# Kernel tuning notes

Hardware: AMD Instinct MI355X
Metric: run time of the kernel (lower is better)

Reference implementation:

```python
import jax, jax.numpy as jnp
import numpy as np

B, S, D_MODEL, D_K, D_V = 8, 2048, 1024, 1024, 1024


def setup_inputs() -> dict:
    key = jax.random.key(0)
    k1, k2, k3, k4 = jax.random.split(key, 4)
    x = jax.random.normal(k1, (B, S, D_MODEL), dtype=jnp.float32)
    # Store projection weights as [d_model, d_out] so projection is x @ W
    # (equivalent to torch Linear(d_model, d_out, bias=False) with W^T).
    scale = 1.0 / np.sqrt(D_MODEL)
    Wq = jax.random.normal(k2, (D_MODEL, D_K), dtype=jnp.float32) * scale
    Wk = jax.random.normal(k3, (D_MODEL, D_K), dtype=jnp.float32) * scale
    Wv = jax.random.normal(k4, (D_MODEL, D_V), dtype=jnp.float32) * scale
    return {"x": x, "Wq": Wq, "Wk": Wk, "Wv": Wv}


def reference(x, Wq, Wk, Wv):
    # Single-head causal self-attention, faithful to the original:
    # NOTE: the original scales by sqrt(x.shape[-1]) == sqrt(d_model),
    # not sqrt(d_k of the projection).
    Q = jnp.einsum('bsd,dk->bsk', x, Wq)
    K = jnp.einsum('bsd,dk->bsk', x, Wk)
    V = jnp.einsum('bsd,dv->bsv', x, Wv)
    inv_scale = 1.0 / jnp.sqrt(jnp.asarray(x.shape[-1], x.dtype))
    A = jnp.einsum('bqk,bsk->bqs', Q, K) * inv_scale  # [B, S, S]
    S_len = A.shape[-1]
    causal = jnp.tril(jnp.ones((S_len, S_len), dtype=bool))  # [S, S]
    A = jnp.where(causal, A, -jnp.inf)
    P = jax.nn.softmax(A, axis=-1)
    return jnp.einsum('bqs,bsv->bqv', P, V)
```

## Files before the change

kernel.cpp:

```cpp
#include <hip/hip_runtime.h>
#include <hip/hip_bf16.h>
#include <stdint.h>


typedef __bf16 bf16_t;
typedef __bf16 bf16x4 __attribute__((ext_vector_type(4)));
typedef __bf16 bf16x8 __attribute__((ext_vector_type(8)));
typedef float  floatx4 __attribute__((ext_vector_type(4)));

#define NB 8
#define SS 2048
#define DD 1024
#define INV_SCALE 0.03125f

__device__ __forceinline__ void async_ld16(const void* g, void* l) {
  __builtin_amdgcn_global_load_lds(
      (const __attribute__((address_space(1))) void*)g,
      (__attribute__((address_space(3))) void*)l, 16, 0, 0);
}

__device__ __forceinline__ void mm_core(const bf16_t* __restrict__ Ab,
                                        const bf16_t* __restrict__ Bb,
                                        int lda, int ldb, int kTiles,
                                        bf16_t* sA, bf16_t* sB,
                                        floatx4 acc[4][4]) {
  const int t    = threadIdx.x;
  const int lane = t & 63;
  const int wm   = (t >> 6) >> 1;
  const int wn   = (t >> 6) & 1;
  const int fm   = lane & 15;
  const int q    = lane >> 4;
  const int xo   = fm & 7;

  const bf16_t* ga[4]; const bf16_t* gb[4];
  bf16_t* la[4]; bf16_t* lb[4];
#pragma unroll
  for (int k = 0; k < 4; ++k) {
    const int u   = k * 256 + t;
    const int row = u >> 3;
    const int cc  = (u & 7) ^ (row & 7);
    ga[k] = Ab + (size_t)row * lda + cc * 8;
    gb[k] = Bb + (size_t)row * ldb + cc * 8;
    la[k] = sA + u * 8;
    lb[k] = sB + u * 8;
  }

  const bf16_t* pa = sA + (wm * 64 + fm) * 64;
  const bf16_t* pb = sB + (wn * 64 + fm) * 64;

  for (int kt = 0; kt < kTiles; ++kt) {
    const int ko = kt * 64;
#pragma unroll
    for (int k = 0; k < 4; ++k) async_ld16(ga[k] + ko, la[k]);
#pragma unroll
    for (int k = 0; k < 4; ++k) async_ld16(gb[k] + ko, lb[k]);
    __syncthreads();
#pragma unroll
    for (int h = 0; h < 2; ++h) {
      const int co = ((h * 4 + q) ^ xo) * 8;
      bf16x8 af[4], bfr[4];
#pragma unroll
      for (int i = 0; i < 4; ++i) af[i]  = *(const bf16x8*)(pa + i * 1024 + co);
#pragma unroll
      for (int j = 0; j < 4; ++j) bfr[j] = *(const bf16x8*)(pb + j * 1024 + co);
#pragma unroll
      for (int i = 0; i < 4; ++i)
#pragma unroll
        for (int j = 0; j < 4; ++j)
          acc[i][j] = __builtin_amdgcn_mfma_f32_16x16x32_bf16(bfr[j], af[i], acc[i][j], 0, 0, 0);
    }
    __syncthreads();
  }
}

__device__ __forceinline__ void zero_acc(floatx4 acc[4][4]) {
#pragma unroll
  for (int i = 0; i < 4; ++i)
#pragma unroll
    for (int j = 0; j < 4; ++j)
      acc[i][j] = floatx4{0.f, 0.f, 0.f, 0.f};
}


__global__ __launch_bounds__(256) void prep(const float* __restrict__ x,
                                            const float* __restrict__ Wq,
                                            const float* __restrict__ Wk,
                                            const float* __restrict__ Wv,
                                            bf16_t* __restrict__ xb,
                                            bf16_t* __restrict__ Wt) {
  __shared__ float tile[32][33];
  const int bid = blockIdx.x;
  const int t = threadIdx.x;
  if (bid < 16384) {
    size_t i = (size_t)bid * 256 + t;
    float4 v = ((const float4*)x)[i];
    bf16x4 o = {(bf16_t)v.x, (bf16_t)v.y, (bf16_t)v.z, (bf16_t)v.w};
    ((bf16x4*)xb)[i] = o;
  } else {
    const int wb = bid - 16384;
    const int z = wb >> 10;
    const int rem = wb & 1023;
    const float* W = (z == 0) ? Wq : (z == 1 ? Wk : Wv);
    bf16_t* O = Wt + (size_t)z * DD * DD;
    const int ty = t >> 3;
    const int tx = t & 7;
    const int k0 = (rem >> 5) * 32, n0 = (rem & 31) * 32;
    float4 v = *(const float4*)(W + (size_t)(k0 + ty) * DD + n0 + tx * 4);
    tile[ty][tx * 4 + 0] = v.x;
    tile[ty][tx * 4 + 1] = v.y;
    tile[ty][tx * 4 + 2] = v.z;
    tile[ty][tx * 4 + 3] = v.w;
    __syncthreads();
    bf16x4 o = {(bf16_t)tile[tx * 4 + 0][ty], (bf16_t)tile[tx * 4 + 1][ty],
                (bf16_t)tile[tx * 4 + 2][ty], (bf16_t)tile[tx * 4 + 3][ty]};
    *(bf16x4*)(O + (size_t)(n0 + ty) * DD + k0 + tx * 4) = o;
  }
}


__global__ __launch_bounds__(256) void qkproj_gemm(
    const bf16_t* __restrict__ xb, const bf16_t* __restrict__ Wt,
    bf16_t* __restrict__ QKb) {
  __shared__ __attribute__((aligned(16))) bf16_t sA[128 * 64];
  __shared__ __attribute__((aligned(16))) bf16_t sB[128 * 64];
  const int mt = blockIdx.x, nt = blockIdx.y;
  const bf16_t* Ab = xb + (size_t)mt * 128 * DD;
  const bf16_t* Bb = Wt + (size_t)nt * 128 * DD;
  bf16_t* Cb = QKb + (size_t)mt * 128 * (2 * DD) + nt * 128;
  floatx4 acc[4][4];
  zero_acc(acc);
  mm_core(Ab, Bb, DD, DD, DD / 64, sA, sB, acc);
  const int lane = threadIdx.x & 63;
  const int wm = (threadIdx.x >> 6) >> 1, wn = (threadIdx.x >> 6) & 1;
  const int m0 = wm * 64 + (lane & 15);
  const int n0 = wn * 64 + (lane >> 4) * 4;
#pragma unroll
  for (int i = 0; i < 4; ++i)
#pragma unroll
    for (int j = 0; j < 4; ++j) {
      floatx4 a = acc[i][j];
      bf16x4 o = {(bf16_t)a[0], (bf16_t)a[1], (bf16_t)a[2], (bf16_t)a[3]};
      *(bf16x4*)(Cb + (size_t)(m0 + i * 16) * (2 * DD) + n0 + j * 16) = o;
    }
}


__global__ __launch_bounds__(256) void vproj_gemm(
    const bf16_t* __restrict__ xb, const bf16_t* __restrict__ Wt,
    bf16_t* __restrict__ VtB) {
  __shared__ __attribute__((aligned(16))) bf16_t sA[128 * 64];
  __shared__ __attribute__((aligned(16))) bf16_t sB[128 * 64];
  const int bid = blockIdx.x;
  const int nb = bid & 127;
  const int m  = bid >> 7;
  const int n  = nb & 15;
  const int b  = nb >> 4;
  const bf16_t* Ab = Wt + (size_t)2 * DD * DD + (size_t)m * 128 * DD;
  const bf16_t* Bb = xb + (size_t)b * SS * DD + (size_t)n * 128 * DD;
  bf16_t* Cb = VtB + (size_t)b * DD * SS + (size_t)m * 128 * SS + n * 128;
  floatx4 acc[4][4];
  zero_acc(acc);
  mm_core(Ab, Bb, DD, DD, DD / 64, sA, sB, acc);
  const int lane = threadIdx.x & 63;
  const int wm = (threadIdx.x >> 6) >> 1, wn = (threadIdx.x >> 6) & 1;
  const int m0 = wm * 64 + (lane & 15);
  const int n0 = wn * 64 + (lane >> 4) * 4;
#pragma unroll
  for (int i = 0; i < 4; ++i)
#pragma unroll
    for (int j = 0; j < 4; ++j) {
      floatx4 a = acc[i][j];
      bf16x4 o = {(bf16_t)a[0], (bf16_t)a[1], (bf16_t)a[2], (bf16_t)a[3]};
      *(bf16x4*)(Cb + (size_t)(m0 + i * 16) * SS + n0 + j * 16) = o;
    }
}


__global__ __launch_bounds__(256) void qk_p(
    const bf16_t* __restrict__ Q, const bf16_t* __restrict__ K,
    bf16_t* __restrict__ P, float* __restrict__ lpart) {
  const int b  = blockIdx.x & 7;
  const int tt = 135 - (blockIdx.x >> 3);
  int qi = (int)((sqrtf(8.0f * tt + 1.0f) - 1.0f) * 0.5f);
  while ((qi + 1) * (qi + 2) / 2 <= tt) ++qi;
  while (qi * (qi + 1) / 2 > tt) --qi;
  const int ki = tt - qi * (qi + 1) / 2;

  __shared__ __attribute__((aligned(16))) bf16_t sA[128 * 64];
  __shared__ __attribute__((aligned(16))) bf16_t sB[128 * 64];
  __shared__ float reds[2][128];
  const bf16_t* Ab = Q + ((size_t)b * SS + qi * 128) * (size_t)(2 * DD);
  const bf16_t* Bb = K + ((size_t)b * SS + ki * 128) * (size_t)(2 * DD);
  floatx4 acc[4][4];
  zero_acc(acc);
  mm_core(Ab, Bb, 2 * DD, 2 * DD, DD / 64, sA, sB, acc);

  const int lane = threadIdx.x & 63;
  const int wm = (threadIdx.x >> 6) >> 1, wn = (threadIdx.x >> 6) & 1;
  const bool diag = (ki == qi);
  bf16_t* Pb = P + (size_t)b * SS * SS;
  const int qloc0 = wm * 64 + (lane & 15);
  const int kvb0  = wn * 64 + (lane >> 4) * 4;

#pragma unroll
  for (int i = 0; i < 4; ++i) {
    const int qrow = qloc0 + i * 16;
    float partial = 0.f;
#pragma unroll
    for (int j = 0; j < 4; ++j) {
      const int kvb = kvb0 + j * 16;
      floatx4 p;
#pragma unroll
      for (int r = 0; r < 4; ++r) {
        const float s = acc[i][j][r] * INV_SCALE;
        p[r] = (diag && (kvb + r) > qrow) ? 0.f : __expf(s);
        partial += p[r];
      }
      bf16x4 o = {(bf16_t)p[0], (bf16_t)p[1], (bf16_t)p[2], (bf16_t)p[3]};
      *(bf16x4*)(Pb + (size_t)(qi * 128 + qrow) * SS + ki * 128 + kvb) = o;
    }
    partial += __shfl_xor(partial, 16);
    partial += __shfl_xor(partial, 32);
    if ((lane >> 4) == 0) reds[wn][qrow] = partial;
  }
  __syncthreads();
  const int t = threadIdx.x;
  if (t < 128) {
    size_t row = (size_t)b * SS + qi * 128 + t;
    lpart[row * 16 + ki] = reds[0][t] + reds[1][t];
  }
}


__global__ __launch_bounds__(256) void pv_gemm(
    const bf16_t* __restrict__ P, const bf16_t* __restrict__ Vt,
    const float* __restrict__ lpart, float* __restrict__ Out) {
  const int bid = blockIdx.x;
  const int b  = bid & 7;
  const int nj = (bid >> 3) & 7;
  const int qi = 15 - (bid >> 6);

  __shared__ __attribute__((aligned(16))) bf16_t sA[128 * 64];
  __shared__ __attribute__((aligned(16))) bf16_t sB[128 * 64];
  __shared__ float sRl[128];
  const int t = threadIdx.x;
  if (t < 128) {
    const float* lp = lpart + ((size_t)b * SS + qi * 128 + t) * 16;
    float L = 0.f;
    for (int ci = 0; ci <= qi; ++ci) L += lp[ci];
    sRl[t] = 1.0f / L;
  }
  const bf16_t* Ab = P + (size_t)b * SS * SS + (size_t)qi * 128 * SS;
  const bf16_t* Bb = Vt + (size_t)b * DD * SS + (size_t)nj * 128 * SS;
  float* Cb = Out + (size_t)b * SS * DD + (size_t)qi * 128 * DD + nj * 128;
  floatx4 acc[4][4];
  zero_acc(acc);
  mm_core(Ab, Bb, SS, SS, (qi + 1) * 2, sA, sB, acc);
  const int lane = threadIdx.x & 63;
  const int wm = (threadIdx.x >> 6) >> 1, wn = (threadIdx.x >> 6) & 1;
  const int m0 = wm * 64 + (lane & 15);
  const int n0 = wn * 64 + (lane >> 4) * 4;
#pragma unroll
  for (int i2 = 0; i2 < 4; ++i2) {
    const float scale = sRl[m0 + i2 * 16];
    float* crow = Cb + (size_t)(m0 + i2 * 16) * DD + n0;
#pragma unroll
    for (int j = 0; j < 4; ++j) {
      floatx4 o = acc[i2][j];
      o[0] *= scale; o[1] *= scale; o[2] *= scale; o[3] *= scale;
      *(floatx4*)(crow + j * 16) = o;
    }
  }
}


extern "C" void kernel_launch(void* const* d_in, const int* in_sizes, int n_in,
                              void* d_out, int out_size, void* d_ws, size_t ws_size,
                              hipStream_t stream) {
  const float* x  = (const float*)d_in[0];
  const float* Wq = (const float*)d_in[1];
  const float* Wk = (const float*)d_in[2];
  const float* Wv = (const float*)d_in[3];
  float* out = (float*)d_out;

  char* ws = (char*)d_ws;
  bf16_t* xb   = (bf16_t*)(ws);
  bf16_t* Wt   = (bf16_t*)(ws + 33554432ull);
  bf16_t* QKb  = (bf16_t*)(ws + 39845888ull);
  bf16_t* VtB  = (bf16_t*)(ws + 106954752ull);
  bf16_t* Pb   = (bf16_t*)(ws + 140509184ull);
  float*  lpart= (float*)(ws + 207618048ull);
  (void)in_sizes; (void)n_in; (void)out_size; (void)ws_size;

  prep<<<16384 + 3072, 256, 0, stream>>>(x, Wq, Wk, Wv, xb, Wt);
  qkproj_gemm<<<dim3(128, 16), 256, 0, stream>>>(xb, Wt, QKb);
  vproj_gemm<<<1024, 256, 0, stream>>>(xb, Wt, VtB);
  qk_p<<<1088, 256, 0, stream>>>(QKb, QKb + DD, Pb, lpart);
  pv_gemm<<<1024, 256, 0, stream>>>(Pb, VtB, lpart, out);
}
```

Measured before the change: 378.4 us.

## Use 256x256 tiled GEMM core with 4-stage async pipeline for projections

```diff
diff --git a/kernel.cpp b/kernel.cpp
--- a/kernel.cpp
+++ b/kernel.cpp
@@ -17,6 +17,108 @@
   __builtin_amdgcn_global_load_lds(
       (const __attribute__((address_space(1))) void*)g,
       (__attribute__((address_space(3))) void*)l, 16, 0, 0);
+}
+
+__device__ __forceinline__ void mm256_core(const bf16_t* __restrict__ Ab,
+                                           const bf16_t* __restrict__ Bb,
+                                           int lda, int ldb, int nt,
+                                           bf16_t* sA, bf16_t* sB,
+                                           floatx4 acc[8][4]) {
+  const int t    = threadIdx.x;
+  const int lane = t & 63;
+  const int wid  = t >> 6;
+  const int wm   = wid >> 2;
+  const int wn   = wid & 3;
+  const int fm   = lane & 15;
+  const int q    = lane >> 4;
+  const int co   = (q ^ ((fm >> 1) & 3)) * 8;
+
+  size_t goA[2], goB[2]; int lo[2];
+#pragma unroll
+  for (int k = 0; k < 2; ++k) {
+    const int u   = k * 512 + t;
+    const int row = u >> 2;
+    const int cg  = (u & 3) ^ ((row >> 1) & 3);
+    goA[k] = (size_t)row * lda + cg * 8;
+    goB[k] = (size_t)row * ldb + cg * 8;
+    lo[k]  = u * 8;
+  }
+
+  auto stage = [&](int tile) {
+    bf16_t* la = sA + (tile & 3) * 8192;
+    bf16_t* lb = sB + (tile & 3) * 8192;
+    const size_t ko = (size_t)tile * 32;
+    async_ld16(Ab + ko + goA[0], la + lo[0]);
+    async_ld16(Ab + ko + goA[1], la + lo[1]);
+    async_ld16(Bb + ko + goB[0], lb + lo[0]);
+    async_ld16(Bb + ko + goB[1], lb + lo[1]);
+  };
+
+  stage(0);
+  if (nt > 1) stage(1);
+  if (nt > 2) stage(2);
+
+  const int paOff = (wm * 128 + fm) * 32;
+  const int pbOff = (wn * 64 + fm) * 32;
+
+  for (int kt = 0; kt < nt; ++kt) {
+    if (kt + 3 < nt) {
+      stage(kt + 3);
+      asm volatile("s_waitcnt vmcnt(12)" ::: "memory");
+    } else if (kt + 2 < nt) {
+      asm volatile("s_waitcnt vmcnt(8)" ::: "memory");
+    } else if (kt + 1 < nt) {
+      asm volatile("s_waitcnt vmcnt(4)" ::: "memory");
+    } else {
+      asm volatile("s_waitcnt vmcnt(0)" ::: "memory");
+    }
+    __builtin_amdgcn_s_barrier();
+    asm volatile("" ::: "memory");
+
+    const bf16_t* pa = sA + (kt & 3) * 8192 + paOff;
+    const bf16_t* pb = sB + (kt & 3) * 8192 + pbOff;
+    bf16x8 af[8], bv[4];
+#pragma unroll
+    for (int j = 0; j < 4; ++j) bv[j] = *(const bf16x8*)(pb + j * 512 + co);
+#pragma unroll
+    for (int i = 0; i < 8; ++i) af[i] = *(const bf16x8*)(pa + i * 512 + co);
+
+    __builtin_amdgcn_s_setprio(1);
+#pragma unroll
+    for (int i = 0; i < 8; ++i)
+#pragma unroll
+      for (int j = 0; j < 4; ++j)
+        acc[i][j] = __builtin_amdgcn_mfma_f32_16x16x32_bf16(bv[j], af[i], acc[i][j], 0, 0, 0);
+    __builtin_amdgcn_s_setprio(0);
+
+    asm volatile("" ::: "memory");
+    __builtin_amdgcn_s_barrier();
+  }
+}
+
+__device__ __forceinline__ void zero_acc8(floatx4 acc[8][4]) {
+#pragma unroll
+  for (int i = 0; i < 8; ++i)
+#pragma unroll
+    for (int j = 0; j < 4; ++j)
+      acc[i][j] = floatx4{0.f, 0.f, 0.f, 0.f};
+}
+
+__device__ __forceinline__ void store_c256_bf16(bf16_t* __restrict__ Cb, int ldc,
+                                                floatx4 acc[8][4]) {
+  const int lane = threadIdx.x & 63;
+  const int wid  = threadIdx.x >> 6;
+  const int wm = wid >> 2, wn = wid & 3;
+  const int m0 = wm * 128 + (lane & 15);
+  const int n0 = wn * 64 + (lane >> 4) * 4;
+#pragma unroll
+  for (int i = 0; i < 8; ++i)
+#pragma unroll
+    for (int j = 0; j < 4; ++j) {
+      floatx4 a = acc[i][j];
+      bf16x4 o = {(bf16_t)a[0], (bf16_t)a[1], (bf16_t)a[2], (bf16_t)a[3]};
+      *(bf16x4*)(Cb + (size_t)(m0 + i * 16) * ldc + n0 + j * 16) = o;
+    }
 }
 
 __device__ __forceinline__ void mm_core(const bf16_t* __restrict__ Ab,
@@ -118,61 +220,38 @@
 }
 
 
-__global__ __launch_bounds__(256) void qkproj_gemm(
+__global__ __launch_bounds__(512, 2) void qkproj_gemm(
     const bf16_t* __restrict__ xb, const bf16_t* __restrict__ Wt,
     bf16_t* __restrict__ QKb) {
-  __shared__ __attribute__((aligned(16))) bf16_t sA[128 * 64];
-  __shared__ __attribute__((aligned(16))) bf16_t sB[128 * 64];
+  __shared__ __attribute__((aligned(16))) bf16_t sA[4 * 8192];
+  __shared__ __attribute__((aligned(16))) bf16_t sB[4 * 8192];
   const int mt = blockIdx.x, nt = blockIdx.y;
-  const bf16_t* Ab = xb + (size_t)mt * 128 * DD;
-  const bf16_t* Bb = Wt + (size_t)nt * 128 * DD;
-  bf16_t* Cb = QKb + (size_t)mt * 128 * (2 * DD) + nt * 128;
-  floatx4 acc[4][4];
-  zero_acc(acc);
-  mm_core(Ab, Bb, DD, DD, DD / 64, sA, sB, acc);
-  const int lane = threadIdx.x & 63;
-  const int wm = (threadIdx.x >> 6) >> 1, wn = (threadIdx.x >> 6) & 1;
-  const int m0 = wm * 64 + (lane & 15);
-  const int n0 = wn * 64 + (lane >> 4) * 4;
-#pragma unroll
-  for (int i = 0; i < 4; ++i)
-#pragma unroll
-    for (int j = 0; j < 4; ++j) {
-      floatx4 a = acc[i][j];
-      bf16x4 o = {(bf16_t)a[0], (bf16_t)a[1], (bf16_t)a[2], (bf16_t)a[3]};
-      *(bf16x4*)(Cb + (size_t)(m0 + i * 16) * (2 * DD) + n0 + j * 16) = o;
-    }
-}
-
-
-__global__ __launch_bounds__(256) void vproj_gemm(
+  const bf16_t* Ab = xb + (size_t)mt * 256 * DD;
+  const bf16_t* Bb = Wt + (size_t)nt * 256 * DD;
+  bf16_t* Cb = QKb + (size_t)mt * 256 * (2 * DD) + nt * 256;
+  floatx4 acc[8][4];
+  zero_acc8(acc);
+  mm256_core(Ab, Bb, DD, DD, DD / 32, sA, sB, acc);
+  store_c256_bf16(Cb, 2 * DD, acc);
+}
+
+
+__global__ __launch_bounds__(512, 2) void vproj_gemm(
     const bf16_t* __restrict__ xb, const bf16_t* __restrict__ Wt,
     bf16_t* __restrict__ VtB) {
-  __shared__ __attribute__((aligned(16))) bf16_t sA[128 * 64];
-  __shared__ __attribute__((aligned(16))) bf16_t sB[128 * 64];
+  __shared__ __attribute__((aligned(16))) bf16_t sA[4 * 8192];
+  __shared__ __attribute__((aligned(16))) bf16_t sB[4 * 8192];
   const int bid = blockIdx.x;
-  const int nb = bid & 127;
-  const int m  = bid >> 7;
-  const int n  = nb & 15;
-  const int b  = nb >> 4;
-  const bf16_t* Ab = Wt + (size_t)2 * DD * DD + (size_t)m * 128 * DD;
-  const bf16_t* Bb = xb + (size_t)b * SS * DD + (size_t)n * 128 * DD;
-  bf16_t* Cb = VtB + (size_t)b * DD * SS + (size_t)m * 128 * SS + n * 128;
-  floatx4 acc[4][4];
-  zero_acc(acc);
-  mm_core(Ab, Bb, DD, DD, DD / 64, sA, sB, acc);
-  const int lane = threadIdx.x & 63;
-  const int wm = (threadIdx.x >> 6) >> 1, wn = (threadIdx.x >> 6) & 1;
-  const int m0 = wm * 64 + (lane & 15);
-  const int n0 = wn * 64 + (lane >> 4) * 4;
-#pragma unroll
-  for (int i = 0; i < 4; ++i)
-#pragma unroll
-    for (int j = 0; j < 4; ++j) {
-      floatx4 a = acc[i][j];
-      bf16x4 o = {(bf16_t)a[0], (bf16_t)a[1], (bf16_t)a[2], (bf16_t)a[3]};
-      *(bf16x4*)(Cb + (size_t)(m0 + i * 16) * SS + n0 + j * 16) = o;
-    }
+  const int n = bid & 7;
+  const int m = (bid >> 3) & 3;
+  const int b = bid >> 5;
+  const bf16_t* Ab = Wt + (size_t)2 * DD * DD + (size_t)m * 256 * DD;
+  const bf16_t* Bb = xb + (size_t)b * SS * DD + (size_t)n * 256 * DD;
+  bf16_t* Cb = VtB + (size_t)b * DD * SS + (size_t)m * 256 * SS + n * 256;
+  floatx4 acc[8][4];
+  zero_acc8(acc);
+  mm256_core(Ab, Bb, DD, DD, DD / 32, sA, sB, acc);
+  store_c256_bf16(Cb, SS, acc);
 }
 
 
@@ -293,8 +372,8 @@
   (void)in_sizes; (void)n_in; (void)out_size; (void)ws_size;
 
   prep<<<16384 + 3072, 256, 0, stream>>>(x, Wq, Wk, Wv, xb, Wt);
-  qkproj_gemm<<<dim3(128, 16), 256, 0, stream>>>(xb, Wt, QKb);
-  vproj_gemm<<<1024, 256, 0, stream>>>(xb, Wt, VtB);
+  qkproj_gemm<<<dim3(64, 8), 512, 0, stream>>>(xb, Wt, QKb);
+  vproj_gemm<<<256, 512, 0, stream>>>(xb, Wt, VtB);
   qk_p<<<1088, 256, 0, stream>>>(QKb, QKb + DD, Pb, lpart);
   pv_gemm<<<1024, 256, 0, stream>>>(Pb, VtB, lpart, out);
 }
```

After: 371.7 us. No clear change (-1.8%).
